# Optimization experiments

Measured on AMD Instinct MI355X. Metric: run time of the kernel, lower is better.

The kernel has to match this reference:

```python
import jax, jax.numpy as jnp
import numpy as np

B, IN_CH, OUT_CH, HEADS, DIM_HEAD, R = 8, 512, 256, 8, 32, 16
H1, W1, H2, W2 = 32, 32, 64, 64
EPS_BN, EPS_LN = 1e-5, 1e-6

# relative position index table (static, as in RelativePositionBias.__init__)
_c = np.stack(np.meshgrid(np.arange(R), np.arange(R), indexing='ij')).reshape(2, -1)
_rel = (_c[:, :, None] - _c[:, None, :]).transpose(1, 2, 0)
_rel[:, :, 0] += R - 1
_rel[:, :, 1] += R - 1
_rel[:, :, 0] *= 2 * R - 1
REL_IDX = jnp.asarray(_rel.sum(-1).reshape(-1))  # [(R*R)*(R*R)]


def _conv(t, w, groups=1, pad=0):
    return jax.lax.conv_general_dilated(t, w, (1, 1), [(pad, pad), (pad, pad)], feature_group_count=groups)


def _dsconv(t, dw, pw):
    # depthwise 3x3 (pad 1) followed by pointwise 1x1, both bias-free
    return _conv(_conv(t, dw, groups=t.shape[1], pad=1), pw)


def _bn(t, g, b):
    # BatchNorm2d in training mode: batch statistics over (B,H,W)
    m = t.mean((0, 2, 3), keepdims=True)
    v = ((t - m) ** 2).mean((0, 2, 3), keepdims=True)
    return (t - m) * jax.lax.rsqrt(v + EPS_BN) * g[None, :, None, None] + b[None, :, None, None]


def _ln_heads(t, g, b):
    # per-head LayerNorm over dim_head; t: [B, heads, N, d], g/b: [heads, d]
    m = t.mean(-1, keepdims=True)
    v = ((t - m) ** 2).mean(-1, keepdims=True)
    return (t - m) * jax.lax.rsqrt(v + EPS_LN) * g[None, :, None, :] + b[None, :, None, :]


def _resize_bilinear(t, Ho, Wo):
    # F.interpolate(mode='bilinear', align_corners=True) on NCHW
    _, _, Hc, Wc = t.shape
    ys = jnp.linspace(0.0, Hc - 1.0, Ho)
    xs = jnp.linspace(0.0, Wc - 1.0, Wo)
    y0 = jnp.floor(ys).astype(jnp.int32); y1 = jnp.clip(y0 + 1, 0, Hc - 1); wy = (ys - y0)[:, None]
    x0 = jnp.floor(xs).astype(jnp.int32); x1 = jnp.clip(x0 + 1, 0, Wc - 1); wx = xs - x0
    rows = t[:, :, y0, :] * (1.0 - wy) + t[:, :, y1, :] * wy
    return rows[:, :, :, x0] * (1.0 - wx) + rows[:, :, :, x1] * wx


def _split_heads(t):
    # 'b (dim_head heads) h w -> b heads (h w) dim_head'
    b, _, h, w = t.shape
    return t.reshape(b, DIM_HEAD, HEADS, h, w).transpose(0, 2, 3, 4, 1).reshape(b, HEADS, h * w, DIM_HEAD)


def reference(x1, x2, conv_ch_w, conv_ch_b, norm_l_g, norm_l_b, norm_h_g, norm_h_b,
              to_kv_dw, to_kv_pw, to_q_dw, to_q_pw, to_out_dw, to_out_pw,
              rel_table, normq_g, normq_b, normk_g, normk_b, norm2_g, norm2_b, mlp_w):
    # channel-change 1x1 conv + upsampled residual
    x1c = _conv(x1, conv_ch_w) + conv_ch_b[None, :, None, None]
    residue = _resize_bilinear(x1c, H2, W2)
    x1n = _bn(x1, norm_l_g, norm_l_b)
    x2n = _bn(x2, norm_h_g, norm_h_b)
    # cross attention: K,V from low-res x1, Q from high-res x2
    kv = _dsconv(x1n, to_kv_dw, to_kv_pw)          # [B, 2*OUT_CH, H1, W1]
    k, v = kv[:, :OUT_CH], kv[:, OUT_CH:]
    q = _dsconv(x2n, to_q_dw, to_q_pw)             # [B, OUT_CH, H2, W2]
    k = _resize_bilinear(k, R, R)
    v = _resize_bilinear(v, R, R)
    q = _ln_heads(_split_heads(q), normq_g, normq_b)   # [B,H,H2*W2,d]
    k = _ln_heads(_split_heads(k), normk_g, normk_b)   # [B,H,R*R,d]
    v = _split_heads(v)
    attn = jnp.einsum('bhid,bhjd->bhij', q, k)
    bias = rel_table[REL_IDX].reshape(R, R, R * R, HEADS)
    bias = jnp.repeat(jnp.repeat(bias, H2 // R, axis=0), W2 // R, axis=1)
    bias = bias.reshape(H2 * W2, R * R, HEADS).transpose(2, 0, 1)[None]
    attn = (attn + bias) * (1.0 / DIM_HEAD)            # softmax-free scaling
    o = jnp.einsum('bhij,bhjd->bhid', attn, v)
    o = o.reshape(B, HEADS, H2, W2, DIM_HEAD).transpose(0, 4, 1, 2, 3).reshape(B, OUT_CH, H2, W2)
    o = _dsconv(o, to_out_dw, to_out_pw)
    o = o + residue
    res2 = o
    o = jax.nn.relu(_bn(o, norm2_g, norm2_b))
    return _conv(o, mlp_w) + res2


def setup_inputs() -> dict:
    key = jax.random.key(0)
    ks = jax.random.split(key, 16)
    W = 0.02  # conv-weight init scale
    return {
        'x1': jax.random.normal(ks[0], (B, IN_CH, H1, W1), jnp.float32),
        'x2': jax.random.normal(ks[1], (B, OUT_CH, H2, W2), jnp.float32),
        'conv_ch_w': jax.random.normal(ks[2], (OUT_CH, IN_CH, 1, 1), jnp.float32) * W,
        'conv_ch_b': jnp.zeros((OUT_CH,), jnp.float32),
        'norm_l_g': jnp.ones((IN_CH,), jnp.float32),
        'norm_l_b': jnp.zeros((IN_CH,), jnp.float32),
        'norm_h_g': jnp.ones((OUT_CH,), jnp.float32),
        'norm_h_b': jnp.zeros((OUT_CH,), jnp.float32),
        'to_kv_dw': jax.random.normal(ks[3], (IN_CH, 1, 3, 3), jnp.float32) * W,
        'to_kv_pw': jax.random.normal(ks[4], (2 * OUT_CH, IN_CH, 1, 1), jnp.float32) * W,
        'to_q_dw': jax.random.normal(ks[5], (OUT_CH, 1, 3, 3), jnp.float32) * W,
        'to_q_pw': jax.random.normal(ks[6], (OUT_CH, OUT_CH, 1, 1), jnp.float32) * W,
        'to_out_dw': jax.random.normal(ks[7], (OUT_CH, 1, 3, 3), jnp.float32) * W,
        'to_out_pw': jax.random.normal(ks[8], (OUT_CH, OUT_CH, 1, 1), jnp.float32) * W,
        'rel_table': jax.random.normal(ks[9], ((2 * R - 1) * (2 * R - 1), HEADS), jnp.float32) * 0.02,
        'normq_g': jnp.ones((HEADS, DIM_HEAD), jnp.float32),
        'normq_b': jnp.zeros((HEADS, DIM_HEAD), jnp.float32),
        'normk_g': jnp.ones((HEADS, DIM_HEAD), jnp.float32),
        'normk_b': jnp.zeros((HEADS, DIM_HEAD), jnp.float32),
        'norm2_g': jnp.ones((OUT_CH,), jnp.float32),
        'norm2_b': jnp.zeros((OUT_CH,), jnp.float32),
        'mlp_w': jax.random.normal(ks[10], (OUT_CH, OUT_CH, 1, 1), jnp.float32) * W,
    }
```

## Files before the change

kernel.cpp:

```cpp
#include <hip/hip_runtime.h>
#include <math.h>

#define NB_   8
#define INCH  512
#define OUTCH 256
#define NHEAD 8
#define DHEAD 32

typedef __attribute__((ext_vector_type(8))) short short8v;
typedef __attribute__((ext_vector_type(4))) short short4v;
typedef __attribute__((ext_vector_type(4))) float f32x4;

__device__ inline short f2bf(float f) {
    unsigned u = __float_as_uint(f);
    unsigned r = u + 0x7FFFu + ((u >> 16) & 1u);
    return (short)(r >> 16);
}

__global__ void pack_w(const float* __restrict__ W, short* __restrict__ Wp, int Co, int Ci) {
    const int idx = blockIdx.x * 256 + threadIdx.x;
    if (idx >= Co * Ci) return;
    const int m = idx / Ci, i = idx % Ci;
    const int kt = i >> 5, w32 = i & 31;
    const int h = w32 >> 4, q = (w32 & 15) >> 2, r = w32 & 3;
    Wp[m * Ci + kt * 32 + q * 8 + h * 4 + r] = f2bf(W[idx]);
}

template <int BN_RELU>
__global__ __launch_bounds__(256, 4)
void pack_tile(const float* __restrict__ in, const float* __restrict__ scale,
               const float* __restrict__ shift, short* __restrict__ outp, int C, int P) {
    __shared__ float s[32][256];
    const int tid = threadIdx.x;
    const int p0 = blockIdx.x * 256;
    const int kt = blockIdx.y;
    const int b  = blockIdx.z;
#pragma unroll
    for (int c = 0; c < 32; ++c) {
        const int gc = kt * 32 + c;
        float v = in[((size_t)b * C + gc) * P + p0 + tid];
        if (BN_RELU) {
            v = v * scale[gc] + shift[gc];
            v = v > 0.f ? v : 0.f;
        }
        s[c][tid] = v;
    }
    __syncthreads();
    short* op = outp + ((size_t)b * P + p0 + tid) * C + kt * 32;
#pragma unroll
    for (int q = 0; q < 4; ++q) {
        short8v v;
#pragma unroll
        for (int h = 0; h < 2; ++h)
#pragma unroll
            for (int r = 0; r < 4; ++r)
                v[h * 4 + r] = f2bf(s[h * 16 + q * 4 + r][tid]);
        *reinterpret_cast<short8v*>(op + q * 8) = v;
    }
}

template <int W_>
__global__ __launch_bounds__(256, 4)
void dw3_direct(const float* __restrict__ in, const float* __restrict__ scale,
                const float* __restrict__ shift, const float* __restrict__ dw,
                short* __restrict__ outp, int C, int H) {
    constexpr int XG = W_ / 8;
    constexpr int RT = 256 / W_;
    __shared__ __align__(16) short so[256][40];
    const int tid = threadIdx.x;
    const int cg  = tid & 7;
    const int pxg = tid >> 3;
    const int row = pxg / XG;
    const int xg  = pxg % XG;
    const int x0  = xg * 8;
    const int y   = blockIdx.x * RT + row;
    const int kt  = blockIdx.y;
    const int b   = blockIdx.z;
    const int P   = H * W_;

    float acc[4][8];
#pragma unroll
    for (int r = 0; r < 4; ++r)
#pragma unroll
        for (int j = 0; j < 8; ++j) acc[r][j] = 0.f;

#pragma unroll
    for (int r = 0; r < 4; ++r) {
        const int gc = kt * 32 + cg * 4 + r;
        const float sc = scale ? scale[gc] : 1.f;
        const float sh = scale ? shift[gc] : 0.f;
        const float* wp = dw + gc * 9;
#pragma unroll
        for (int dy = 0; dy < 3; ++dy) {
            const int gy = y - 1 + dy;
            if (gy < 0 || gy >= H) continue;
            const float* bp = in + ((size_t)b * C + gc) * P + gy * W_;
            float w[10];
            w[0] = (x0 > 0) ? bp[x0 - 1] : 0.f;
            const float4 m0 = *reinterpret_cast<const float4*>(bp + x0);
            const float4 m1 = *reinterpret_cast<const float4*>(bp + x0 + 4);
            w[1] = m0.x; w[2] = m0.y; w[3] = m0.z; w[4] = m0.w;
            w[5] = m1.x; w[6] = m1.y; w[7] = m1.z; w[8] = m1.w;
            w[9] = (x0 + 8 < W_) ? bp[x0 + 8] : 0.f;
            if (scale) {
#pragma unroll
                for (int t = 0; t < 10; ++t) w[t] = w[t] * sc + sh;
                if (x0 == 0) w[0] = 0.f;
                if (x0 + 8 >= W_) w[9] = 0.f;
            }
            const float t0 = wp[dy * 3 + 0], t1 = wp[dy * 3 + 1], t2 = wp[dy * 3 + 2];
#pragma unroll
            for (int j = 0; j < 8; ++j)
                acc[r][j] += t0 * w[j] + t1 * w[j + 1] + t2 * w[j + 2];
        }
    }

    const int posb = (cg & 3) * 8 + (cg >> 2) * 4;
#pragma unroll
    for (int j = 0; j < 8; ++j) {
        short4v v;
#pragma unroll
        for (int r = 0; r < 4; ++r) v[r] = f2bf(acc[r][j]);
        *reinterpret_cast<short4v*>(&so[pxg * 8 + j][posb]) = v;
    }
    __syncthreads();
    short* op = outp + ((size_t)b * P + blockIdx.x * 256 + tid) * C + kt * 32;
#pragma unroll
    for (int q = 0; q < 4; ++q)
        *reinterpret_cast<short8v*>(op + q * 8) = *reinterpret_cast<const short8v*>(&so[tid][q * 8]);
}

template <int HAS_RES>
__global__ __launch_bounds__(256, 4)
void mfma_pw(const short* __restrict__ Xp, const short* __restrict__ Wp,
             const float* __restrict__ bias, const float* __restrict__ res,
             float* __restrict__ out, int Ci, int Co, int P) {
    __shared__ short Ash[4096];
    __shared__ short Bsh[2048];
    const int b   = blockIdx.z;
    const int m0  = blockIdx.y * 128;
    const int n0  = blockIdx.x * 64;
    const int tid = threadIdx.x;
    const int lane = tid & 63;
    const int wid  = tid >> 6;
    const int wr = wid >> 1, wc = wid & 1;
    const int ql = lane >> 4, l16 = lane & 15;

    f32x4 acc[4][2];
#pragma unroll
    for (int mb = 0; mb < 4; ++mb)
#pragma unroll
        for (int nb = 0; nb < 2; ++nb) acc[mb][nb] = (f32x4){0.f, 0.f, 0.f, 0.f};

    const int sm_ = tid & 127;
    const int sq_ = tid >> 7;
    const int bn_ = tid & 63;
    const int bq_ = tid >> 6;

    const size_t wrow = (size_t)(m0 + sm_) * Ci;
    const size_t xrow = ((size_t)b * P + n0 + bn_) * Ci;

    const int nkt = Ci >> 5;
    for (int kt = 0; kt < nkt; ++kt) {
        const int kof = kt * 32;
#pragma unroll
        for (int r = 0; r < 2; ++r) {
            const int q = r * 2 + sq_;
            __builtin_amdgcn_global_load_lds(Wp + wrow + kof + q * 8, &Ash[r * 2048 + tid * 8], 16, 0, 0);
        }
        __builtin_amdgcn_global_load_lds(Xp + xrow + kof + bq_ * 8, &Bsh[tid * 8], 16, 0, 0);
        __syncthreads();

        short8v a[4], bf[2];
#pragma unroll
        for (int mb = 0; mb < 4; ++mb)
            a[mb] = *reinterpret_cast<const short8v*>(&Ash[ql * 1024 + (wr * 64 + mb * 16 + l16) * 8]);
#pragma unroll
        for (int nb = 0; nb < 2; ++nb)
            bf[nb] = *reinterpret_cast<const short8v*>(&Bsh[ql * 512 + (wc * 32 + nb * 16 + l16) * 8]);
#pragma unroll
        for (int mb = 0; mb < 4; ++mb)
#pragma unroll
            for (int nb = 0; nb < 2; ++nb)
                acc[mb][nb] = __builtin_amdgcn_mfma_f32_16x16x32_bf16(a[mb], bf[nb], acc[mb][nb], 0, 0, 0);
        __syncthreads();
    }

#pragma unroll
    for (int mb = 0; mb < 4; ++mb) {
        const int row = m0 + wr * 64 + mb * 16 + ql * 4;
#pragma unroll
        for (int nb = 0; nb < 2; ++nb) {
            const int col = n0 + wc * 32 + nb * 16 + l16;
            const size_t base = ((size_t)b * Co + row) * P + col;
#pragma unroll
            for (int j = 0; j < 4; ++j) {
                float v = acc[mb][nb][j];
                if (bias) v += bias[row + j];
                if (HAS_RES) v += res[base + (size_t)j * P];
                out[base + (size_t)j * P] = v;
            }
        }
    }
}

template <int C, int Hi, int Wi, int Ho, int Wo>
__global__ void resize_bilinear(const float* __restrict__ in, float* __restrict__ out, int ibs) {
    const int idx = blockIdx.x * 256 + threadIdx.x;
    const int x = idx & (Wo - 1);
    const int y = (idx / Wo) & (Ho - 1);
    const int c = (idx / (Wo * Ho)) & (C - 1);
    const int b = idx / (Wo * Ho * C);
    const float fy = (float)y * (float)(Hi - 1) / (float)(Ho - 1);
    const float fx = (float)x * (float)(Wi - 1) / (float)(Wo - 1);
    int y0 = (int)floorf(fy); int y1 = min(y0 + 1, Hi - 1); const float wy = fy - (float)y0;
    int x0 = (int)floorf(fx); int x1 = min(x0 + 1, Wi - 1); const float wx = fx - (float)x0;
    const float* pc = in + (size_t)b * ibs + (size_t)c * Hi * Wi;
    const float r0 = pc[y0 * Wi + x0] * (1.f - wx) + pc[y0 * Wi + x1] * wx;
    const float r1 = pc[y1 * Wi + x0] * (1.f - wx) + pc[y1 * Wi + x1] * wx;
    out[idx] = r0 * (1.f - wy) + r1 * wy;
}

__global__ __launch_bounds__(256, 8)
void bn_stats_part(const float* __restrict__ in, float* __restrict__ part, int C, int HW) {
    const int b = blockIdx.x;
    const int c = blockIdx.y;
    const float* p = in + ((size_t)b * C + c) * HW;
    float s1 = 0.f, s2 = 0.f;
    for (int i = threadIdx.x * 4; i < HW; i += 1024) {
        const float4 v = *reinterpret_cast<const float4*>(p + i);
        s1 += v.x + v.y + v.z + v.w;
        s2 += v.x * v.x + v.y * v.y + v.z * v.z + v.w * v.w;
    }
#pragma unroll
    for (int o = 32; o >= 1; o >>= 1) {
        s1 += __shfl_xor(s1, o);
        s2 += __shfl_xor(s2, o);
    }
    __shared__ float sh1[4], sh2[4];
    if ((threadIdx.x & 63) == 0) { sh1[threadIdx.x >> 6] = s1; sh2[threadIdx.x >> 6] = s2; }
    __syncthreads();
    if (threadIdx.x == 0) {
        part[((size_t)c * gridDim.x + b) * 2 + 0] = sh1[0] + sh1[1] + sh1[2] + sh1[3];
        part[((size_t)c * gridDim.x + b) * 2 + 1] = sh2[0] + sh2[1] + sh2[2] + sh2[3];
    }
}

__global__ void bn_finish(const float* __restrict__ part, const float* __restrict__ g,
                          const float* __restrict__ bt, float* __restrict__ scale,
                          float* __restrict__ shift, int C, int HW, float eps) {
    const int c = blockIdx.x * 256 + threadIdx.x;
    if (c >= C) return;
    float s1 = 0.f, s2 = 0.f;
#pragma unroll
    for (int b = 0; b < NB_; ++b) {
        s1 += part[((size_t)c * NB_ + b) * 2 + 0];
        s2 += part[((size_t)c * NB_ + b) * 2 + 1];
    }
    const float invN = 1.f / (float)(NB_ * HW);
    const float m = s1 * invN;
    const float var = s2 * invN - m * m;
    const float sc = g[c] * rsqrtf(var + eps);
    scale[c] = sc;
    shift[c] = bt[c] - m * sc;
}

__global__ void ln_split(const float* __restrict__ in, const float* __restrict__ g,
                         const float* __restrict__ bt, float* __restrict__ out,
                         int HW, int applyLN, float eps) {
    const int row = blockIdx.x * 8 + (threadIdx.x >> 5);
    const int d = threadIdx.x & 31;
    const int j = row % HW;
    const int h = (row / HW) % NHEAD;
    const int b = row / (HW * NHEAD);
    float v = in[((size_t)b * OUTCH + d * NHEAD + h) * HW + j];
    if (applyLN) {
        float s1 = v, s2 = v * v;
#pragma unroll
        for (int o = 16; o >= 1; o >>= 1) {
            s1 += __shfl_xor(s1, o, 32);
            s2 += __shfl_xor(s2, o, 32);
        }
        const float m = s1 * (1.f / 32.f);
        const float var = s2 * (1.f / 32.f) - m * m;
        v = (v - m) * rsqrtf(var + eps) * g[h * 32 + d] + bt[h * 32 + d];
    }
    out[((size_t)(b * NHEAD + h) * HW + j) * 32 + d] = v;
}

__global__ void kv_outer(const float* __restrict__ kn, const float* __restrict__ vh,
                         float* __restrict__ M) {
    __shared__ float vs[256][32];
    const int bh = blockIdx.x;
    const float* kp = kn + (size_t)bh * 256 * 32;
    const float* vp = vh + (size_t)bh * 256 * 32;
    const int tid = threadIdx.y * 32 + threadIdx.x;
    for (int t = tid; t < 256 * 32; t += 1024) vs[t >> 5][t & 31] = vp[t];
    __syncthreads();
    const int e = threadIdx.x, dd = threadIdx.y;
    float acc = 0.f;
    for (int j = 0; j < 256; ++j) acc += kp[j * 32 + e] * vs[j][dd];
    M[((size_t)bh * 32 + e) * 32 + dd] = acc;
}

__global__ void bias_v(const float* __restrict__ rel, const float* __restrict__ vh,
                       float* __restrict__ Bv) {
    const int gid = blockIdx.x * 8 + (threadIdx.x >> 5);
    const int d = threadIdx.x & 31;
    const int qb = gid % 256;
    const int h = (gid / 256) % NHEAD;
    const int b = gid / (256 * NHEAD);
    const int qy = qb >> 4, qx = qb & 15;
    const float* vp = vh + (size_t)(b * NHEAD + h) * 256 * 32;
    float acc = 0.f;
    for (int j = 0; j < 256; ++j) {
        const int ky = j >> 4, kx = j & 15;
        const float bias = rel[((qy - ky + 15) * 31 + (qx - kx + 15)) * NHEAD + h];
        acc += bias * vp[j * 32 + d];
    }
    Bv[((size_t)(b * NHEAD + h) * 256 + qb) * 32 + d] = acc;
}

__global__ __launch_bounds__(256, 2)
void attn_out(const float* __restrict__ q, const float* __restrict__ gq,
              const float* __restrict__ bq, const float* __restrict__ M,
              const float* __restrict__ Bv, float* __restrict__ o) {
    const int gid = blockIdx.x * 256 + threadIdx.x;
    const int ip = (gid & 2047) * 2;
    const int h  = (gid >> 11) & 7;
    const int b  = gid >> 14;

    const float* Mp = M + ((size_t)(b * NHEAD + h) << 10);
    {
        uint64_t a = (uint64_t)Mp;
        uint32_t lo = __builtin_amdgcn_readfirstlane((uint32_t)a);
        uint32_t hi = __builtin_amdgcn_readfirstlane((uint32_t)(a >> 32));
        Mp = (const float*)((((uint64_t)hi) << 32) | lo);
    }

    const float* qp = q + (size_t)b * OUTCH * 4096 + h * 4096 + ip;
    float q0[32], q1[32];
    float a1 = 0.f, a2 = 0.f, b1 = 0.f, b2 = 0.f;
#pragma unroll
    for (int d = 0; d < 32; ++d) {
        const float2 v = *reinterpret_cast<const float2*>(qp + (size_t)d * NHEAD * 4096);
        q0[d] = v.x; q1[d] = v.y;
        a1 += v.x; a2 += v.x * v.x;
        b1 += v.y; b2 += v.y * v.y;
    }
    {
        const float m0 = a1 * (1.f / 32.f);
        const float r0 = rsqrtf(a2 * (1.f / 32.f) - m0 * m0 + 1e-6f);
        const float m1 = b1 * (1.f / 32.f);
        const float r1 = rsqrtf(b2 * (1.f / 32.f) - m1 * m1 + 1e-6f);
#pragma unroll
        for (int d = 0; d < 32; ++d) {
            const float gg = gq[h * 32 + d], bb = bq[h * 32 + d];
            q0[d] = (q0[d] - m0) * r0 * gg + bb;
            q1[d] = (q1[d] - m1) * r1 * gg + bb;
        }
    }

    const int y = ip >> 6, x = ip & 63;
    const int qb0 = (y >> 2) * 16 + (x >> 2);
    const int qb1 = (y >> 2) * 16 + ((x + 1) >> 2);
    const float* Bp0 = Bv + (((size_t)(b * NHEAD + h) * 256 + qb0) << 5);
    const float* Bp1 = Bv + (((size_t)(b * NHEAD + h) * 256 + qb1) << 5);
    float acc0[32], acc1[32];
#pragma unroll
    for (int t = 0; t < 8; ++t) {
        const float4 v0 = *reinterpret_cast<const float4*>(Bp0 + t * 4);
        const float4 v1 = *reinterpret_cast<const float4*>(Bp1 + t * 4);
        acc0[t * 4 + 0] = v0.x; acc0[t * 4 + 1] = v0.y; acc0[t * 4 + 2] = v0.z; acc0[t * 4 + 3] = v0.w;
        acc1[t * 4 + 0] = v1.x; acc1[t * 4 + 1] = v1.y; acc1[t * 4 + 2] = v1.z; acc1[t * 4 + 3] = v1.w;
    }

    for (int e = 0; e < 32; ++e) {
        const float qe0 = q0[e], qe1 = q1[e];
#pragma unroll
        for (int d = 0; d < 32; ++d) {
            const float m = Mp[e * 32 + d];
            acc0[d] += qe0 * m;
            acc1[d] += qe1 * m;
        }
    }

    float* op = o + (size_t)b * OUTCH * 4096 + h * 4096 + ip;
#pragma unroll
    for (int d = 0; d < 32; ++d) {
        float2 v;
        v.x = acc0[d] * (1.f / 32.f);
        v.y = acc1[d] * (1.f / 32.f);
        *reinterpret_cast<float2*>(op + (size_t)d * NHEAD * 4096) = v;
    }
}

extern "C" void kernel_launch(void* const* d_in, const int* in_sizes, int n_in,
                              void* d_out, int out_size, void* d_ws, size_t ws_size,
                              hipStream_t stream) {
    const float* x1        = (const float*)d_in[0];
    const float* x2        = (const float*)d_in[1];
    const float* conv_ch_w = (const float*)d_in[2];
    const float* conv_ch_b = (const float*)d_in[3];
    const float* norm_l_g  = (const float*)d_in[4];
    const float* norm_l_b  = (const float*)d_in[5];
    const float* norm_h_g  = (const float*)d_in[6];
    const float* norm_h_b  = (const float*)d_in[7];
    const float* to_kv_dw  = (const float*)d_in[8];
    const float* to_kv_pw  = (const float*)d_in[9];
    const float* to_q_dw   = (const float*)d_in[10];
    const float* to_q_pw   = (const float*)d_in[11];
    const float* to_out_dw = (const float*)d_in[12];
    const float* to_out_pw = (const float*)d_in[13];
    const float* rel_table = (const float*)d_in[14];
    const float* normq_g   = (const float*)d_in[15];
    const float* normq_b   = (const float*)d_in[16];
    const float* normk_g   = (const float*)d_in[17];
    const float* normk_b   = (const float*)d_in[18];
    const float* norm2_g   = (const float*)d_in[19];
    const float* norm2_b   = (const float*)d_in[20];
    const float* mlp_w     = (const float*)d_in[21];
    float* Dout = (float*)d_out;

    float* ws = (float*)d_ws;
    const size_t NBIG = (size_t)NB_ * OUTCH * 4096;
    float* RES = ws;
    float* A   = ws + NBIG;
    float* Bb  = ws + 2 * NBIG;
    float* sm  = ws + 3 * NBIG;
    float* scale1 = sm;            float* shift1 = sm + 512;
    float* scale2 = sm + 1024;     float* shift2 = sm + 1280;
    float* scale3 = sm + 1536;     float* shift3 = sm + 1792;
    float* k16 = sm + 2048;
    float* v16 = k16 + 524288;
    float* kn  = v16 + 524288;
    float* vh  = kn  + 524288;
    float* Mm  = vh  + 524288;
    float* Bv  = Mm  + 65536;
    short* Wq  = (short*)(Bv + 524288);
    short* Wo  = Wq + 65536;
    short* Wm  = Wo + 65536;
    short* Wc  = Wm + 65536;
    short* Wkv = Wc + 131072;
    float* bnpart = (float*)(Wkv + 262144);

    short* Xp1 = (short*)Bb;
    short* Xp2 = (short*)Bb + 4194304;
    short* Xp  = (short*)Bb;
    float* kv  = A;

    pack_w<<<256, 256, 0, stream>>>(to_q_pw, Wq, 256, 256);
    pack_w<<<256, 256, 0, stream>>>(to_out_pw, Wo, 256, 256);
    pack_w<<<256, 256, 0, stream>>>(mlp_w, Wm, 256, 256);
    pack_w<<<512, 256, 0, stream>>>(conv_ch_w, Wc, 256, 512);
    pack_w<<<1024, 256, 0, stream>>>(to_kv_pw, Wkv, 512, 512);

    pack_tile<0><<<dim3(4, 16, 8), 256, 0, stream>>>(x1, nullptr, nullptr, Xp1, 512, 1024);
    mfma_pw<0><<<dim3(16, 2, 8), 256, 0, stream>>>(Xp1, Wc, conv_ch_b, nullptr, A, 512, 256, 1024);
    resize_bilinear<256, 32, 32, 64, 64><<<32768, 256, 0, stream>>>(A, RES, 256 * 1024);
    bn_stats_part<<<dim3(8, 512), 256, 0, stream>>>(x1, bnpart, 512, 1024);
    bn_finish<<<2, 256, 0, stream>>>(bnpart, norm_l_g, norm_l_b, scale1, shift1, 512, 1024, 1e-5f);
    dw3_direct<32><<<dim3(4, 16, 8), 256, 0, stream>>>(x1, scale1, shift1, to_kv_dw, Xp2, 512, 32);
    mfma_pw<0><<<dim3(16, 4, 8), 256, 0, stream>>>(Xp2, Wkv, nullptr, nullptr, kv, 512, 512, 1024);
    resize_bilinear<256, 32, 32, 16, 16><<<2048, 256, 0, stream>>>(kv, k16, 512 * 1024);
    resize_bilinear<256, 32, 32, 16, 16><<<2048, 256, 0, stream>>>(kv + 256 * 1024, v16, 512 * 1024);
    bn_stats_part<<<dim3(8, 256), 256, 0, stream>>>(x2, bnpart, 256, 4096);
    bn_finish<<<1, 256, 0, stream>>>(bnpart, norm_h_g, norm_h_b, scale2, shift2, 256, 4096, 1e-5f);
    dw3_direct<64><<<dim3(16, 8, 8), 256, 0, stream>>>(x2, scale2, shift2, to_q_dw, Xp, 256, 64);
    mfma_pw<0><<<dim3(64, 2, 8), 256, 0, stream>>>(Xp, Wq, nullptr, nullptr, A, 256, 256, 4096);
    ln_split<<<2048, 256, 0, stream>>>(k16, normk_g, normk_b, kn, 256, 1, 1e-6f);
    ln_split<<<2048, 256, 0, stream>>>(v16, nullptr, nullptr, vh, 256, 0, 0.f);
    kv_outer<<<64, dim3(32, 32), 0, stream>>>(kn, vh, Mm);
    bias_v<<<2048, 256, 0, stream>>>(rel_table, vh, Bv);
    attn_out<<<512, 256, 0, stream>>>(A, normq_g, normq_b, Mm, Bv, A);
    dw3_direct<64><<<dim3(16, 8, 8), 256, 0, stream>>>(A, nullptr, nullptr, to_out_dw, Xp, 256, 64);
    mfma_pw<1><<<dim3(64, 2, 8), 256, 0, stream>>>(Xp, Wo, nullptr, RES, A, 256, 256, 4096);
    bn_stats_part<<<dim3(8, 256), 256, 0, stream>>>(A, bnpart, 256, 4096);
    bn_finish<<<1, 256, 0, stream>>>(bnpart, norm2_g, norm2_b, scale3, shift3, 256, 4096, 1e-5f);
    pack_tile<1><<<dim3(16, 8, 8), 256, 0, stream>>>(A, scale3, shift3, Xp, 256, 4096);
    mfma_pw<1><<<dim3(64, 2, 8), 256, 0, stream>>>(Xp, Wm, nullptr, A, Dout, 256, 256, 4096);
}
```

Before: 347.0 us.

## Compute relative-position bias times V as a batched bf16 MFMA GEMM

Replaces the scalar bias_v kernel, which rebuilt the relative-position bias on the fly for every (query, key) pair, with a precomputed bf16 bias matrix per head. V is transposed and packed per head. The existing MFMA pointwise GEMM, extended with per-batch weight offsets, then computes bias·V, and attn_out reads Bv in the new [h][qb][b*32+d] layout. This trades a heavy scalar loop over 256 keys for two small packing kernels plus a tensor-core GEMM, at the cost of bf16 precision on the bias and V.

```diff
diff --git a/kernel.cpp b/kernel.cpp
--- a/kernel.cpp
+++ b/kernel.cpp
@@ -24,6 +24,40 @@
     const int kt = i >> 5, w32 = i & 31;
     const int h = w32 >> 4, q = (w32 & 15) >> 2, r = w32 & 3;
     Wp[m * Ci + kt * 32 + q * 8 + h * 4 + r] = f2bf(W[idx]);
+}
+
+__global__ void bias_mat(const float* __restrict__ rel, short* __restrict__ Bm) {
+    const int idx = blockIdx.x * 256 + threadIdx.x;
+    const int h  = idx >> 16;
+    const int qb = (idx >> 8) & 255;
+    const int pp = idx & 255;
+    const int kt = pp >> 5, w = pp & 31;
+    const int q = w >> 3, hh = (w >> 2) & 1, r = w & 3;
+    const int j = kt * 32 + hh * 16 + q * 4 + r;
+    const int qy = qb >> 4, qx = qb & 15;
+    const int ky = j >> 4, kx = j & 15;
+    Bm[idx] = f2bf(rel[((qy - ky + 15) * 31 + (qx - kx + 15)) * NHEAD + h]);
+}
+
+__global__ void pack_vT(const float* __restrict__ v16, short* __restrict__ Xpv) {
+    const int h = blockIdx.x;
+    const int b = blockIdx.y;
+    const int tid = threadIdx.x;
+#pragma unroll
+    for (int cc = 0; cc < 4; ++cc) {
+        const int c  = tid * 4 + cc;
+        const int d  = c >> 5;
+        const int ck = c & 31;
+        const int kt = ck >> 2, q = ck & 3;
+        const float* vp = v16 + ((size_t)(b * 256 + d * NHEAD + h)) * 256;
+        short8v v;
+#pragma unroll
+        for (int hh = 0; hh < 2; ++hh)
+#pragma unroll
+            for (int r = 0; r < 4; ++r)
+                v[hh * 4 + r] = f2bf(vp[kt * 32 + hh * 16 + q * 4 + r]);
+        *reinterpret_cast<short8v*>(&Xpv[(size_t)h * 65536 + (b * 32 + d) * 256 + kt * 32 + q * 8]) = v;
+    }
 }
 
 template <int BN_RELU>
@@ -130,7 +164,7 @@
         *reinterpret_cast<short8v*>(op + q * 8) = *reinterpret_cast<const short8v*>(&so[tid][q * 8]);
 }
 
-template <int HAS_RES>
+template <int HAS_RES, int BATCH_W>
 __global__ __launch_bounds__(256, 4)
 void mfma_pw(const short* __restrict__ Xp, const short* __restrict__ Wp,
              const float* __restrict__ bias, const float* __restrict__ res,
@@ -157,7 +191,7 @@
     const int bn_ = tid & 63;
     const int bq_ = tid >> 6;
 
-    const size_t wrow = (size_t)(m0 + sm_) * Ci;
+    const size_t wrow = (size_t)(m0 + sm_) * Ci + (BATCH_W ? (size_t)b * Co * Ci : 0);
     const size_t xrow = ((size_t)b * P + n0 + bn_) * Ci;
 
     const int nkt = Ci >> 5;
@@ -303,24 +337,6 @@
     M[((size_t)bh * 32 + e) * 32 + dd] = acc;
 }
 
-__global__ void bias_v(const float* __restrict__ rel, const float* __restrict__ vh,
-                       float* __restrict__ Bv) {
-    const int gid = blockIdx.x * 8 + (threadIdx.x >> 5);
-    const int d = threadIdx.x & 31;
-    const int qb = gid % 256;
-    const int h = (gid / 256) % NHEAD;
-    const int b = gid / (256 * NHEAD);
-    const int qy = qb >> 4, qx = qb & 15;
-    const float* vp = vh + (size_t)(b * NHEAD + h) * 256 * 32;
-    float acc = 0.f;
-    for (int j = 0; j < 256; ++j) {
-        const int ky = j >> 4, kx = j & 15;
-        const float bias = rel[((qy - ky + 15) * 31 + (qx - kx + 15)) * NHEAD + h];
-        acc += bias * vp[j * 32 + d];
-    }
-    Bv[((size_t)(b * NHEAD + h) * 256 + qb) * 32 + d] = acc;
-}
-
 __global__ __launch_bounds__(256, 2)
 void attn_out(const float* __restrict__ q, const float* __restrict__ gq,
               const float* __restrict__ bq, const float* __restrict__ M,
@@ -364,8 +380,8 @@
     const int y = ip >> 6, x = ip & 63;
     const int qb0 = (y >> 2) * 16 + (x >> 2);
     const int qb1 = (y >> 2) * 16 + ((x + 1) >> 2);
-    const float* Bp0 = Bv + (((size_t)(b * NHEAD + h) * 256 + qb0) << 5);
-    const float* Bp1 = Bv + (((size_t)(b * NHEAD + h) * 256 + qb1) << 5);
+    const float* Bp0 = Bv + ((size_t)h * 256 + qb0) * 256 + b * 32;
+    const float* Bp1 = Bv + ((size_t)h * 256 + qb1) * 256 + b * 32;
     float acc0[32], acc1[32];
 #pragma unroll
     for (int t = 0; t < 8; ++t) {
@@ -447,6 +463,8 @@
     short* Xp1 = (short*)Bb;
     short* Xp2 = (short*)Bb + 4194304;
     short* Xp  = (short*)Bb;
+    short* Bmp = (short*)Bb + 8388608;
+    short* Xpv = Bmp + 524288;
     float* kv  = A;
 
     pack_w<<<256, 256, 0, stream>>>(to_q_pw, Wq, 256, 256);
@@ -454,29 +472,31 @@
     pack_w<<<256, 256, 0, stream>>>(mlp_w, Wm, 256, 256);
     pack_w<<<512, 256, 0, stream>>>(conv_ch_w, Wc, 256, 512);
     pack_w<<<1024, 256, 0, stream>>>(to_kv_pw, Wkv, 512, 512);
+    bias_mat<<<2048, 256, 0, stream>>>(rel_table, Bmp);
 
     pack_tile<0><<<dim3(4, 16, 8), 256, 0, stream>>>(x1, nullptr, nullptr, Xp1, 512, 1024);
-    mfma_pw<0><<<dim3(16, 2, 8), 256, 0, stream>>>(Xp1, Wc, conv_ch_b, nullptr, A, 512, 256, 1024);
+    mfma_pw<0, 0><<<dim3(16, 2, 8), 256, 0, stream>>>(Xp1, Wc, conv_ch_b, nullptr, A, 512, 256, 1024);
     resize_bilinear<256, 32, 32, 64, 64><<<32768, 256, 0, stream>>>(A, RES, 256 * 1024);
     bn_stats_part<<<dim3(8, 512), 256, 0, stream>>>(x1, bnpart, 512, 1024);
     bn_finish<<<2, 256, 0, stream>>>(bnpart, norm_l_g, norm_l_b, scale1, shift1, 512, 1024, 1e-5f);
     dw3_direct<32><<<dim3(4, 16, 8), 256, 0, stream>>>(x1, scale1, shift1, to_kv_dw, Xp2, 512, 32);
-    mfma_pw<0><<<dim3(16, 4, 8), 256, 0, stream>>>(Xp2, Wkv, nullptr, nullptr, kv, 512, 512, 1024);
+    mfma_pw<0, 0><<<dim3(16, 4, 8), 256, 0, stream>>>(Xp2, Wkv, nullptr, nullptr, kv, 512, 512, 1024);
     resize_bilinear<256, 32, 32, 16, 16><<<2048, 256, 0, stream>>>(kv, k16, 512 * 1024);
     resize_bilinear<256, 32, 32, 16, 16><<<2048, 256, 0, stream>>>(kv + 256 * 1024, v16, 512 * 1024);
     bn_stats_part<<<dim3(8, 256), 256, 0, stream>>>(x2, bnpart, 256, 4096);
     bn_finish<<<1, 256, 0, stream>>>(bnpart, norm_h_g, norm_h_b, scale2, shift2, 256, 4096, 1e-5f);
     dw3_direct<64><<<dim3(16, 8, 8), 256, 0, stream>>>(x2, scale2, shift2, to_q_dw, Xp, 256, 64);
-    mfma_pw<0><<<dim3(64, 2, 8), 256, 0, stream>>>(Xp, Wq, nullptr, nullptr, A, 256, 256, 4096);
+    mfma_pw<0, 0><<<dim3(64, 2, 8), 256, 0, stream>>>(Xp, Wq, nullptr, nullptr, A, 256, 256, 4096);
     ln_split<<<2048, 256, 0, stream>>>(k16, normk_g, normk_b, kn, 256, 1, 1e-6f);
     ln_split<<<2048, 256, 0, stream>>>(v16, nullptr, nullptr, vh, 256, 0, 0.f);
+    pack_vT<<<dim3(8, 8), 256, 0, stream>>>(v16, Xpv);
     kv_outer<<<64, dim3(32, 32), 0, stream>>>(kn, vh, Mm);
-    bias_v<<<2048, 256, 0, stream>>>(rel_table, vh, Bv);
+    mfma_pw<0, 1><<<dim3(4, 2, 8), 256, 0, stream>>>(Xpv, Bmp, nullptr, nullptr, Bv, 256, 256, 256);
     attn_out<<<512, 256, 0, stream>>>(A, normq_g, normq_b, Mm, Bv, A);
     dw3_direct<64><<<dim3(16, 8, 8), 256, 0, stream>>>(A, nullptr, nullptr, to_out_dw, Xp, 256, 64);
-    mfma_pw<1><<<dim3(64, 2, 8), 256, 0, stream>>>(Xp, Wo, nullptr, RES, A, 256, 256, 4096);
+    mfma_pw<1, 0><<<dim3(64, 2, 8), 256, 0, stream>>>(Xp, Wo, nullptr, RES, A, 256, 256, 4096);
     bn_stats_part<<<dim3(8, 256), 256, 0, stream>>>(A, bnpart, 256, 4096);
     bn_finish<<<1, 256, 0, stream>>>(bnpart, norm2_g, norm2_b, scale3, shift3, 256, 4096, 1e-5f);
     pack_tile<1><<<dim3(16, 8, 8), 256, 0, stream>>>(A, scale3, shift3, Xp, 256, 4096);
-    mfma_pw<1><<<dim3(64, 2, 8), 256, 0, stream>>>(Xp, Wm, nullptr, A, Dout, 256, 256, 4096);
-}
+    mfma_pw<1, 0><<<dim3(64, 2, 8), 256, 0, stream>>>(Xp, Wm, nullptr, A, Dout, 256, 256, 4096);
+}
```

New measurement: 324.2 us. 6.6% less time.
